# Kernel optimization log

Hardware: AMD Instinct MI355X
Metric: run time of the kernel (lower is better)

The kernel has to match this reference:

```python
import jax, jax.numpy as jnp
import numpy as np

Q_DIM, T_DIM, TOP_M, TEMP = 512, 768, 5, 0.07
B, H, W, K = 8, 64, 64, 128
LN_EPS = 1e-5

def _layernorm(x, g, b):
    mu = jnp.mean(x, axis=-1, keepdims=True)
    var = jnp.mean(jnp.square(x - mu), axis=-1, keepdims=True)
    return (x - mu) * jax.lax.rsqrt(var + LN_EPS) * g + b

def _l2norm(x):
    n = jnp.linalg.norm(x, axis=-1, keepdims=True)
    return x / jnp.maximum(n, 1e-12)

def setup_inputs() -> dict:
    key = jax.random.key(0)
    ks = jax.random.split(key, 12)
    s = lambda d: 1.0 / np.sqrt(d)
    return {
        'visual_features': jax.random.normal(ks[0], (B, H, W, Q_DIM), jnp.float32),
        'text_features': jax.random.normal(ks[1], (B, K, T_DIM), jnp.float32),
        'Wq': jax.random.uniform(ks[2], (Q_DIM, T_DIM), jnp.float32, -s(Q_DIM), s(Q_DIM)),
        'bq': jnp.zeros((T_DIM,), jnp.float32),
        'Wv': jax.random.uniform(ks[3], (T_DIM, Q_DIM), jnp.float32, -s(T_DIM), s(T_DIM)),
        'bv': jnp.zeros((Q_DIM,), jnp.float32),
        'W1': jax.random.uniform(ks[4], (Q_DIM, 4 * Q_DIM), jnp.float32, -s(Q_DIM), s(Q_DIM)),
        'b1': jnp.zeros((4 * Q_DIM,), jnp.float32),
        'W2': jax.random.uniform(ks[5], (4 * Q_DIM, Q_DIM), jnp.float32, -s(4 * Q_DIM), s(4 * Q_DIM)),
        'b2': jnp.zeros((Q_DIM,), jnp.float32),
        'g1': jnp.ones((Q_DIM,), jnp.float32), 'be1': jnp.zeros((Q_DIM,), jnp.float32),
        'g2': jnp.ones((Q_DIM,), jnp.float32), 'be2': jnp.zeros((Q_DIM,), jnp.float32),
    }

def reference(visual_features, text_features, Wq, bq, Wv, bv, W1, b1, W2, b2, g1, be1, g2, be2):
    b, h, w, c = visual_features.shape
    residual = visual_features.reshape(b, h * w, c)
    vis = _layernorm(residual, g1, be1)                      # (B,N,C)
    query = _l2norm(vis @ Wq + bq)                            # (B,N,Ct)
    keyt = _l2norm(text_features)                             # (B,K,Ct)
    value = text_features @ Wv + bv                           # (B,K,C)
    sim = jnp.einsum('bnc,bkc->bnk', query, keyt)             # (B,N,K)
    # top-M sparsification: keep top_m logits, others -> -inf
    top_v = jax.lax.top_k(sim, TOP_M)[0]                      # (B,N,M) sorted desc
    thr = top_v[..., -1:]
    sim = jnp.where(sim >= thr, sim, -jnp.inf)
    attn = jax.nn.softmax(sim / TEMP, axis=-1)
    aligned = jnp.einsum('bnk,bkc->bnc', attn, value)
    fused = residual + aligned
    fused = _layernorm(fused, g2, be2)
    ffn = jax.nn.gelu(fused @ W1 + b1, approximate=False) @ W2 + b2
    out = fused + ffn
    return out.reshape(b, h, w, c)
```

## Files before the change

### kernel.cpp

```cpp
#include <hip/hip_runtime.h>
#include <math.h>

typedef unsigned short u16;
typedef unsigned int   u32;
typedef unsigned long long u64;
typedef __attribute__((ext_vector_type(4))) float f32x4;
typedef __attribute__((ext_vector_type(4))) unsigned int u32x4;
typedef __attribute__((ext_vector_type(8))) _Float16 f16x8;

#define NROWS   32768
#define CDIM    512
#define TDIM    768
#define KKEY    128
#define FFDIM   2048
#define NB      8
#define RPB     4096
#define LN_EPS_ 1e-5f
#define TINV    (1.0f/0.07f)
#define RESCUE_MARGIN 1e-5f

__device__ __forceinline__ u16 f2h(float f){ _Float16 h=(_Float16)f; return __builtin_bit_cast(u16,h); }
__device__ __forceinline__ float h2f(u16 v){ return (float)__builtin_bit_cast(_Float16, v); }
__device__ __forceinline__ unsigned pk2(float a,float b){ return (unsigned)f2h(a)|((unsigned)f2h(b)<<16); }

__device__ __forceinline__ void gl_lds16(const void* g, void* l){
  __builtin_amdgcn_global_load_lds(
      (const __attribute__((address_space(1))) u32*)g,
      (__attribute__((address_space(3))) u32*)l, 16, 0, 0);
}

__device__ __forceinline__ float fast_exp2(float x){
#if __has_builtin(__builtin_amdgcn_exp2f)
  return __builtin_amdgcn_exp2f(x);
#else
  return exp2f(x);
#endif
}
__device__ __forceinline__ float fast_rcp(float x){
#if __has_builtin(__builtin_amdgcn_rcpf)
  return __builtin_amdgcn_rcpf(x);
#else
  return 1.0f/x;
#endif
}

__device__ __forceinline__ float wsumf(float v){
#pragma unroll
  for(int o=1;o<64;o<<=1) v+=__shfl_xor(v,o);
  return v; }
__device__ __forceinline__ float wmaxf(float v){
#pragma unroll
  for(int o=1;o<64;o<<=1) v=fmaxf(v,__shfl_xor(v,o));
  return v; }
__device__ __forceinline__ double wsumd(double v){
#pragma unroll
  for(int o=1;o<64;o<<=1) v+=__shfl_xor(v,o);
  return v; }
__device__ __forceinline__ double wmaxd(double v){
#pragma unroll
  for(int o=1;o<64;o<<=1){ double t=__shfl_xor(v,o); v = t>v ? t : v; }
  return v; }

__device__ __forceinline__ double blocksumd4(double v, double* red){
  const int lane = threadIdx.x & 63, w = threadIdx.x >> 6;
  v = wsumd(v);
  __syncthreads();
  if (lane==0) red[w] = v;
  __syncthreads();
  return red[0]+red[1]+red[2]+red[3];
}

template<int R, int C, bool F16>
__device__ __forceinline__ void tr_tile(const float* __restrict__ in, void* __restrict__ out,
                                        int bx, int by, float (*tile)[33])
{
  int c0 = bx*32, r0 = by*32;
  int tx = threadIdx.x, ty = threadIdx.y;
#pragma unroll
  for (int i=0;i<4;i++){
    int r = r0 + ty + i*8;
    tile[ty+i*8][tx] = in[(size_t)r*C + c0 + tx];
  }
  __syncthreads();
#pragma unroll
  for (int i=0;i<4;i++){
    int cc = c0 + ty + i*8, rr = r0 + tx;
    float v = tile[tx][ty+i*8];
    if (F16) ((u16*)out)[(size_t)cc*R + rr] = f2h(v);
    else     ((float*)out)[(size_t)cc*R + rr] = v;
  }
}

__global__ __launch_bounds__(256) void transpose_all_kernel(
    const float* __restrict__ Wq, const float* __restrict__ W1,
    const float* __restrict__ W2, const float* __restrict__ Wv,
    u16* __restrict__ Wq16t, u16* __restrict__ W116t,
    u16* __restrict__ W216t, float* __restrict__ WvT)
{
  __shared__ float tile[32][33];
  int bid = blockIdx.x;
  if (bid < 384){
    tr_tile<512,768,true>(Wq, Wq16t, bid%24, bid/24, tile);
  } else if (bid < 1408){
    int b = bid-384;  tr_tile<512,2048,true>(W1, W116t, b%64, b/64, tile);
  } else if (bid < 2432){
    int b = bid-1408; tr_tile<2048,512,true>(W2, W216t, b%16, b/16, tile);
  } else {
    int b = bid-2432; tr_tile<768,512,false>(Wv, WvT, b%16, b/16, tile);
  }
}

__global__ __launch_bounds__(256) void keystats_kernel(
    const float* __restrict__ text, const float* __restrict__ bq,
    float* __restrict__ normk, float* __restrict__ crr)
{
  int gw = blockIdx.x*4 + (threadIdx.x>>6);
  int lane = threadIdx.x & 63;
  const float* tr = &text[(size_t)gw*TDIM];
  double ss=0.0, db=0.0;
#pragma unroll
  for (int i=0;i<12;i++){
    float v = tr[lane + 64*i];
    ss += (double)v*(double)v;
    db += (double)bq[lane+64*i]*(double)v;
  }
  ss = wsumd(ss); db = wsumd(db);
  if (lane==0){
    double nk = sqrt(ss); nk = nk>1e-12 ? nk : 1e-12;
    normk[gw] = (float)nk;
    crr[gw]   = (float)db;
  }
}

__global__ __launch_bounds__(256) void ln1_kernel(
    const float* __restrict__ visual, const float* __restrict__ g1, const float* __restrict__ be1,
    float2* __restrict__ musig, u16* __restrict__ vis16)
{
  int row = blockIdx.x*4 + (threadIdx.x>>6);
  int lane = threadIdx.x & 63;
  size_t base = (size_t)row*CDIM + lane*8;
  f32x4 a = *(const f32x4*)&visual[base];
  f32x4 c = *(const f32x4*)&visual[base+4];
  float s = a[0]+a[1]+a[2]+a[3]+c[0]+c[1]+c[2]+c[3];
  s = wsumf(s);
  float mu = s * (1.0f/512.0f);
  float q = 0.f;
#pragma unroll
  for (int i=0;i<4;i++){ float d=a[i]-mu; q+=d*d; }
#pragma unroll
  for (int i=0;i<4;i++){ float d=c[i]-mu; q+=d*d; }
  q = wsumf(q);
  float rs = rsqrtf(q*(1.0f/512.0f) + LN_EPS_);
  int cb = lane*8;
  f32x4 o0,o1;
#pragma unroll
  for (int i=0;i<4;i++) o0[i] = (a[i]-mu)*rs*g1[cb+i]   + be1[cb+i];
#pragma unroll
  for (int i=0;i<4;i++) o1[i] = (c[i]-mu)*rs*g1[cb+4+i] + be1[cb+4+i];
  u32x4 hv;
  hv[0]=pk2(o0[0],o0[1]); hv[1]=pk2(o0[2],o0[3]);
  hv[2]=pk2(o1[0],o1[1]); hv[3]=pk2(o1[2],o1[3]);
  *(u32x4*)&vis16[base] = hv;
  if (lane==0){ float2 ms; ms.x=mu; ms.y=rs; musig[row]=ms; }
}

template<bool LNA>
__global__ __launch_bounds__(256) void gemm_f32_kernel(
    const float* __restrict__ A, const float* __restrict__ Bt, float* __restrict__ C,
    int M, int N, int K, long sA, long sB, long sC,
    const float2* __restrict__ musig, const float* __restrict__ g1, const float* __restrict__ be1)
{
  __shared__ float As[64][17];
  __shared__ float Bs[64][17];
  const int z = blockIdx.z;
  A  += (size_t)z * sA; Bt += (size_t)z * sB; C += (size_t)z * sC;
  const int tid = threadIdx.x;
  const int tx = tid & 15, ty = tid >> 4;
  const int m0 = blockIdx.x*64, n0 = blockIdx.y*64;
  float acc[4][4];
#pragma unroll
  for (int i=0;i<4;i++)
#pragma unroll
    for (int j=0;j<4;j++) acc[i][j]=0.f;
  const int lr = tid >> 2, lc = (tid & 3)*4;
  float2 ms;
  if (LNA) ms = musig[(size_t)z*M + m0 + lr];
  for (int k0=0; k0<K; k0+=16){
    f32x4 av = *(const f32x4*)&A [(size_t)(m0+lr)*K + k0 + lc];
    f32x4 bv = *(const f32x4*)&Bt[(size_t)(n0+lr)*K + k0 + lc];
    if (LNA){
      f32x4 gv  = *(const f32x4*)&g1[k0+lc];
      f32x4 bev = *(const f32x4*)&be1[k0+lc];
#pragma unroll
      for (int i=0;i<4;i++) av[i] = (av[i]-ms.x)*ms.y*gv[i] + bev[i];
    }
#pragma unroll
    for (int i=0;i<4;i++){ As[lr][lc+i]=av[i]; Bs[lr][lc+i]=bv[i]; }
    __syncthreads();
#pragma unroll
    for (int kk=0; kk<16; kk++){
      float a[4], b[4];
#pragma unroll
      for (int i=0;i<4;i++){ a[i]=As[ty*4+i][kk]; b[i]=Bs[tx*4+i][kk]; }
#pragma unroll
      for (int i=0;i<4;i++)
#pragma unroll
        for (int j=0;j<4;j++) acc[i][j] = fmaf(a[i], b[j], acc[i][j]);
    }
    __syncthreads();
  }
#pragma unroll
  for (int i=0;i<4;i++){
    f32x4 o;
#pragma unroll
    for (int j=0;j<4;j++) o[j]=acc[i][j];
    *(f32x4*)&C[(size_t)(m0+ty*4+i)*N + n0 + tx*4] = o;
  }
}

__device__ __forceinline__ float gelu_exact(float v){
  float x  = v*0.70710678118654752440f;
  float ax = fabsf(x);
  float t  = fast_rcp(fmaf(0.3275911f, ax, 1.0f));
  float p  = t*fmaf(t, fmaf(t, fmaf(t, fmaf(t, 1.061405429f, -1.453152027f),
                  1.421413741f), -0.284496736f), 0.254829592f);
  float e  = fast_exp2(ax*ax*(-1.4426950408889634f));
  float y  = 1.0f - p*e;
  float er = (x < 0.0f) ? -y : y;
  return 0.5f*v*(1.0f + er);
}

template<int EPI, int NN, int KK, int NT>
__global__ __launch_bounds__(256) void gemm_f16_kernel(
    const u16* __restrict__ A, const u16* __restrict__ Bt,
    const float* __restrict__ bias,
    float* __restrict__ out_f,
    u16* __restrict__ out_h,
    const u16* __restrict__ add_h)
{
  __shared__ __align__(16) u16 As[128*64];
  __shared__ __align__(16) u16 Bs[128*64];
  const int tid = threadIdx.x;
  const int lane = tid & 63, w = tid >> 6;
  const int wr = w >> 1, wc = w & 1;
  constexpr int NWG = 256*NT;
  const int wg = blockIdx.x;
  const int b2 = (wg & 7)*(NWG/8) + (wg >> 3);
  const int ntile = b2 % NT, mtile = b2 / NT;
  const int m0 = mtile*128, n0 = ntile*128;
  f32x4 acc[4][4];
#pragma unroll
  for (int i=0;i<4;i++)
#pragma unroll
    for (int j=0;j<4;j++) acc[i][j] = (f32x4)0.f;
  const int lr = lane & 15, lk = (lane >> 4)*8;
  const int c8_sw = ((lane & 7) ^ (lane >> 3))*8;
  const size_t stride32 = (size_t)32*KK;
  const u16* aptr = &A [(size_t)(m0 + w*8 + (lane>>3))*KK + c8_sw];
  const u16* bptr = &Bt[(size_t)(n0 + w*8 + (lane>>3))*KK + c8_sw];
  for (int k0=0; k0<KK; k0+=64){
#pragma unroll
    for (int i=0;i<4;i++){
      gl_lds16(aptr + i*stride32, &As[w*512 + i*2048]);
      gl_lds16(bptr + i*stride32, &Bs[w*512 + i*2048]);
    }
    aptr += 64; bptr += 64;
    __syncthreads();
#pragma unroll
    for (int kk=0; kk<64; kk+=32){
      f16x8 af[4], bfv[4];
      const int csw = (kk + lk) ^ ((lr & 7) << 3);
#pragma unroll
      for (int mi=0;mi<4;mi++) af[mi]  = *(const f16x8*)&As[(wr*64 + mi*16 + lr)*64 + csw];
#pragma unroll
      for (int ni=0;ni<4;ni++) bfv[ni] = *(const f16x8*)&Bs[(wc*64 + ni*16 + lr)*64 + csw];
#pragma unroll
      for (int mi=0;mi<4;mi++)
#pragma unroll
        for (int ni=0;ni<4;ni++)
          acc[mi][ni] = __builtin_amdgcn_mfma_f32_16x16x32_f16(af[mi], bfv[ni], acc[mi][ni], 0, 0, 0);
    }
    __syncthreads();
  }
  const int lr4 = (lane >> 4)*4;
  if (EPI == 0){
    float sq[4][4];
#pragma unroll
    for (int mi=0;mi<4;mi++)
#pragma unroll
      for (int r=0;r<4;r++) sq[mi][r]=0.f;
#pragma unroll
    for (int ni=0;ni<4;ni++){
      float bqv = bias[n0 + wc*64 + ni*16 + lr];
#pragma unroll
      for (int mi=0;mi<4;mi++)
#pragma unroll
        for (int r=0;r<4;r++){
          float v = acc[mi][ni][r] + bqv;
          sq[mi][r] += v*v;
        }
    }
#pragma unroll
    for (int o=1;o<16;o<<=1)
#pragma unroll
      for (int mi=0;mi<4;mi++)
#pragma unroll
        for (int r=0;r<4;r++) sq[mi][r] += __shfl_xor(sq[mi][r], o);
    if ((lane & 15) == 0){
      int part = ntile*2 + wc;
#pragma unroll
      for (int mi=0;mi<4;mi++)
#pragma unroll
        for (int r=0;r<4;r++){
          int row = m0 + wr*64 + mi*16 + lr4 + r;
          out_f[(size_t)row*12 + part] = sq[mi][r];
        }
    }
  } else {
    const int row0 = m0 + wr*64 + lr4;
    const int col0 = n0 + wc*64 + lr;
    float bb[4];
#pragma unroll
    for (int ni=0;ni<4;ni++) bb[ni] = bias[col0 + ni*16];
    if (EPI == 1){
      u16* op = out_h + (size_t)row0*NN + col0;
#pragma unroll
      for (int mi=0;mi<4;mi++)
#pragma unroll
        for (int r=0;r<4;r++)
#pragma unroll
          for (int ni=0;ni<4;ni++)
            op[(size_t)(mi*16+r)*NN + ni*16] = f2h(gelu_exact(acc[mi][ni][r] + bb[ni]));
    } else {
      float* op = out_f + (size_t)row0*NN + col0;
      const u16* rp = add_h + (size_t)row0*NN + col0;
#pragma unroll
      for (int mi=0;mi<4;mi++)
#pragma unroll
        for (int r=0;r<4;r++)
#pragma unroll
          for (int ni=0;ni<4;ni++)
            op[(size_t)(mi*16+r)*NN + ni*16] =
                acc[mi][ni][r] + bb[ni] + h2f(rp[(size_t)(mi*16+r)*NN + ni*16]);
    }
  }
}

__global__ __launch_bounds__(256) void rescue_kernel(
    const int* __restrict__ rcnt, const int* __restrict__ rlist,
    const float* __restrict__ visual, const float* __restrict__ text,
    const float* __restrict__ Wq, const float* __restrict__ bq,
    const float* __restrict__ g1, const float* __restrict__ be1,
    const float* __restrict__ g2, const float* __restrict__ be2,
    const float* __restrict__ value, const float* __restrict__ bv,
    u16* __restrict__ fused16)
{
  __shared__ double vis64[512];
  __shared__ double q64[768];
  __shared__ double sims[128];
  __shared__ double pw[128];
  __shared__ double red[4];
  __shared__ double sc2[2];
  __shared__ int klist[128];
  __shared__ int kcount;
  const int tid = threadIdx.x, lane = tid & 63, w = tid >> 6;
  int n = *rcnt; if (n > NROWS) n = NROWS;
  for (int i = blockIdx.x; i < n; i += gridDim.x){
    const int row = rlist[i], b = row >> 12;
    const size_t rb = (size_t)row*CDIM;
    double x0 = (double)visual[rb+tid], x1 = (double)visual[rb+tid+256];
    double s = blocksumd4(x0+x1, red);
    double mu = s*(1.0/512.0);
    double d0 = x0-mu, d1 = x1-mu;
    double var = blocksumd4(d0*d0+d1*d1, red);
    double rs = 1.0/sqrt(var*(1.0/512.0) + 1e-5);
    vis64[tid]     = d0*rs*(double)g1[tid]     + (double)be1[tid];
    vis64[tid+256] = d1*rs*(double)g1[tid+256] + (double)be1[tid+256];
    __syncthreads();
    double qa0=(double)bq[tid], qa1=(double)bq[tid+256], qa2=(double)bq[tid+512];
#pragma unroll 4
    for (int c=0;c<CDIM;c++){
      double v = vis64[c];
      const float* wrow = &Wq[(size_t)c*TDIM];
      qa0 += v*(double)wrow[tid];
      qa1 += v*(double)wrow[tid+256];
      qa2 += v*(double)wrow[tid+512];
    }
    q64[tid]=qa0; q64[tid+256]=qa1; q64[tid+512]=qa2;
    double nq2 = blocksumd4(qa0*qa0+qa1*qa1+qa2*qa2, red);
    double nq = sqrt(nq2); if (nq < 1e-12) nq = 1e-12;
    __syncthreads();
    if (tid < KKEY){
      const float* trow = &text[((size_t)b*KKEY + tid)*TDIM];
      double dot=0.0, nk2=0.0;
#pragma unroll 8
      for (int j=0;j<TDIM;j++){
        double tv = (double)trow[j];
        dot += q64[j]*tv; nk2 += tv*tv;
      }
      double nk = sqrt(nk2); if (nk < 1e-12) nk = 1e-12;
      sims[tid] = dot/(nq*nk);
    }
    __syncthreads();
    if (w == 0){
      double v0=sims[lane], v1=sims[lane+64];
      bool rm0=false, rm1=false;
      double thr=0.0, smax=0.0;
      for (int it=0; it<5; ++it){
        double c0 = rm0 ? -1e300 : v0;
        double c1 = rm1 ? -1e300 : v1;
        double m = wmaxd(c0>c1 ? c0 : c1);
        if (it==0) smax = m;
        thr = m;
        bool h0 = (!rm0) && (v0==m);
        u64 k0 = __ballot(h0);
        if (k0){ if (lane == __ffsll(k0)-1) rm0 = true; }
        else {
          bool h1 = (!rm1) && (v1==m);
          u64 k1 = __ballot(h1);
          if (lane == __ffsll(k1)-1) rm1 = true;
        }
      }
      if (lane==0){ sc2[0]=smax; sc2[1]=thr; kcount=0; }
    }
    __syncthreads();
    const double smax = sc2[0], thr = sc2[1];
    double p = 0.0;
    if (tid < KKEY){
      double sv = sims[tid];
      p = (sv >= thr) ? exp((sv-smax)*(1.0/0.07)) : 0.0;
      pw[tid] = p;
      if (p > 0.0){ int pos = atomicAdd(&kcount, 1); klist[pos] = tid; }
    }
    double Z = blocksumd4(p, red);
    double zi = 1.0/Z;
    __syncthreads();
    double a0=(double)bv[tid], a1=(double)bv[tid+256];
    int kc = kcount;
    for (int ki=0; ki<kc; ++ki){
      int k = klist[ki];
      double wt = pw[k]*zi;
      const float* vr = &value[((size_t)b*KKEY + k)*CDIM];
      a0 += wt*(double)vr[tid];
      a1 += wt*(double)vr[tid+256];
    }
    double f0 = (double)visual[rb+tid]     + a0;
    double f1 = (double)visual[rb+tid+256] + a1;
    double fsum = blocksumd4(f0+f1, red);
    double fmu = fsum*(1.0/512.0);
    double e0=f0-fmu, e1=f1-fmu;
    double fvar = blocksumd4(e0*e0+e1*e1, red);
    double frs = 1.0/sqrt(fvar*(1.0/512.0) + 1e-5);
    fused16[rb+tid]     = f2h((float)(e0*frs*(double)g2[tid]     + (double)be2[tid]));
    fused16[rb+tid+256] = f2h((float)(e1*frs*(double)g2[tid+256] + (double)be2[tid+256]));
    __syncthreads();
  }
}

__global__ __launch_bounds__(256) void attn_ln2_kernel(
    const float* __restrict__ visual,
    const float* __restrict__ tbuf, const float* __restrict__ crr,
    const float* __restrict__ normk, const float* __restrict__ qpart,
    const float* __restrict__ value, const float* __restrict__ bv,
    const float* __restrict__ g2, const float* __restrict__ be2,
    u16* __restrict__ fused16,
    int* __restrict__ rcnt, int* __restrict__ rlist)
{
  const int w = threadIdx.x >> 6, lane = threadIdx.x & 63;
  const int row = blockIdx.x*4 + w;
  const int b = row >> 12;
  float nqp = (lane < 12) ? qpart[(size_t)row*12 + lane] : 0.f;
  float nq2 = wsumf(nqp);
  float nq = fmaxf(sqrtf(nq2), 1e-12f);
  const float* trow = &tbuf[(size_t)row*KKEY];
  float s0 = (trow[lane]    + crr[b*KKEY + lane])    / (nq*normk[b*KKEY + lane]);
  float s1 = (trow[lane+64] + crr[b*KKEY + lane+64]) / (nq*normk[b*KKEY + lane+64]);
  float v0=s0, v1=s1; bool rm0=false, rm1=false;
  float thr=0.f, smax=0.f, m6=0.f;
  for (int it=0; it<6; ++it){
    float c0 = rm0 ? -1e30f : v0;
    float c1 = rm1 ? -1e30f : v1;
    float m = wmaxf(fmaxf(c0,c1));
    if (it==0) smax = m;
    if (it<5){
      thr = m;
      bool h0 = (!rm0) && (v0==m);
      u64 k0 = __ballot(h0);
      if (k0){ if (lane == __ffsll(k0)-1) rm0 = true; }
      else {
        bool h1 = (!rm1) && (v1==m);
        u64 k1 = __ballot(h1);
        if (lane == __ffsll(k1)-1) rm1 = true;
      }
    } else m6 = m;
  }
  if ((thr - m6) < RESCUE_MARGIN){
    if (lane == 0){
      int p = atomicAdd(rcnt, 1);
      rlist[p] = row;
    }
    return;
  }
  float p0 = (s0>=thr) ? expf((s0-smax)*TINV) : 0.f;
  float p1 = (s1>=thr) ? expf((s1-smax)*TINV) : 0.f;
  float Z = wsumf(p0+p1);
  float zi = 1.f/Z;
  float accv[8];
#pragma unroll
  for (int j=0;j<8;j++) accv[j] = bv[lane*8+j];
  u64 mk0 = __ballot(p0>0.f);
  u64 mk1 = __ballot(p1>0.f);
  while (mk0){
    int l = __ffsll(mk0)-1; mk0 &= mk0-1;
    float wt = __shfl(p0, l)*zi;
    const f32x4* vr = (const f32x4*)&value[((size_t)b*KKEY + l)*CDIM + lane*8];
    f32x4 va = vr[0], vb = vr[1];
#pragma unroll
    for (int j=0;j<4;j++){ accv[j] += wt*va[j]; accv[4+j] += wt*vb[j]; }
  }
  while (mk1){
    int l = __ffsll(mk1)-1; mk1 &= mk1-1;
    float wt = __shfl(p1, l)*zi;
    const f32x4* vr = (const f32x4*)&value[((size_t)b*KKEY + l + 64)*CDIM + lane*8];
    f32x4 va = vr[0], vb = vr[1];
#pragma unroll
    for (int j=0;j<4;j++){ accv[j] += wt*va[j]; accv[4+j] += wt*vb[j]; }
  }
  size_t rb = (size_t)row*CDIM + lane*8;
  f32x4 r0v = *(const f32x4*)&visual[rb];
  f32x4 r1v = *(const f32x4*)&visual[rb+4];
  float f[8];
#pragma unroll
  for (int j=0;j<4;j++){ f[j]=r0v[j]+accv[j]; f[4+j]=r1v[j]+accv[4+j]; }
  float fs=0.f;
#pragma unroll
  for (int j=0;j<8;j++) fs += f[j];
  fs = wsumf(fs);
  float fmu = fs*(1.0f/512.0f);
  float fvv=0.f;
#pragma unroll
  for (int j=0;j<8;j++){ float d=f[j]-fmu; fvv+=d*d; }
  fvv = wsumf(fvv);
  float frs = rsqrtf(fvv*(1.0f/512.0f) + LN_EPS_);
  int cb = lane*8;
  f32x4 o0,o1;
#pragma unroll
  for (int j=0;j<4;j++) o0[j] = (f[j]-fmu)*frs*g2[cb+j]     + be2[cb+j];
#pragma unroll
  for (int j=0;j<4;j++) o1[j] = (f[4+j]-fmu)*frs*g2[cb+4+j] + be2[cb+4+j];
  u32x4 hv;
  hv[0]=pk2(o0[0],o0[1]); hv[1]=pk2(o0[2],o0[3]);
  hv[2]=pk2(o1[0],o1[1]); hv[3]=pk2(o1[2],o1[3]);
  *(u32x4*)&fused16[rb] = hv;
}

extern "C" void kernel_launch(void* const* d_in, const int* in_sizes, int n_in,
                              void* d_out, int out_size, void* d_ws, size_t ws_size,
                              hipStream_t stream)
{
  (void)in_sizes; (void)n_in; (void)out_size; (void)ws_size;
  const float* visual = (const float*)d_in[0];
  const float* text   = (const float*)d_in[1];
  const float* Wq     = (const float*)d_in[2];
  const float* bq     = (const float*)d_in[3];
  const float* Wv     = (const float*)d_in[4];
  const float* bv     = (const float*)d_in[5];
  const float* W1     = (const float*)d_in[6];
  const float* b1     = (const float*)d_in[7];
  const float* W2     = (const float*)d_in[8];
  const float* b2     = (const float*)d_in[9];
  const float* g1     = (const float*)d_in[10];
  const float* be1    = (const float*)d_in[11];
  const float* g2     = (const float*)d_in[12];
  const float* be2    = (const float*)d_in[13];
  float* out = (float*)d_out;

  char* ws = (char*)d_ws;
  size_t off = 0;
  auto alloc = [&](size_t bytes)->char*{
    char* p = ws + off; off += (bytes + 255) & ~(size_t)255; return p; };

  u16*    vis16  = (u16*)   alloc((size_t)NROWS*CDIM*2);
  u16*    h16    = (u16*)   alloc((size_t)NROWS*FFDIM*2);
  float*  tbuf   = (float*) alloc((size_t)NROWS*KKEY*4);
  float*  Mrt    = (float*) alloc((size_t)NB*KKEY*CDIM*4);
  float*  value  = (float*) alloc((size_t)NB*KKEY*CDIM*4);
  u16*    Wq16t  = (u16*)   alloc((size_t)TDIM*CDIM*2);
  u16*    W116t  = (u16*)   alloc((size_t)FFDIM*CDIM*2);
  u16*    W216t  = (u16*)   alloc((size_t)CDIM*FFDIM*2);
  float*  WvT    = (float*) alloc((size_t)CDIM*TDIM*4);
  float*  qpart  = (float*) alloc((size_t)NROWS*12*4);
  float*  normk  = (float*) alloc((size_t)NB*KKEY*4);
  float*  crr    = (float*) alloc((size_t)NB*KKEY*4);
  float2* musig  = (float2*)alloc((size_t)NROWS*8);
  int*    rcnt   = (int*)   alloc(256);
  int*    rlist  = (int*)   alloc((size_t)NROWS*4);
  u16*    fused16 = vis16;

  hipMemsetAsync(rcnt, 0, sizeof(int), stream);

  transpose_all_kernel<<<2816, dim3(32,8), 0, stream>>>(
      Wq, W1, W2, Wv, Wq16t, W116t, W216t, WvT);
  keystats_kernel<<<256, 256, 0, stream>>>(text, bq, normk, crr);
  gemm_f32_kernel<false><<<dim3(2, 8, 8), 256, 0, stream>>>(
      text, Wq, Mrt, KKEY, CDIM, TDIM, (long)KKEY*TDIM, 0, (long)KKEY*CDIM,
      nullptr, nullptr, nullptr);
  gemm_f32_kernel<false><<<dim3(2, 8, 8), 256, 0, stream>>>(
      text, WvT, value, KKEY, CDIM, TDIM, (long)KKEY*TDIM, 0, (long)KKEY*CDIM,
      nullptr, nullptr, nullptr);
  ln1_kernel<<<NROWS/4, 256, 0, stream>>>(visual, g1, be1, musig, vis16);
  gemm_f32_kernel<true><<<dim3(64, 2, 8), 256, 0, stream>>>(
      visual, Mrt, tbuf, RPB, KKEY, CDIM, (long)RPB*CDIM, (long)KKEY*CDIM, (long)RPB*KKEY,
      musig, g1, be1);
  gemm_f16_kernel<0,TDIM,CDIM,6><<<1536, 256, 0, stream>>>(
      vis16, Wq16t, bq, qpart, nullptr, nullptr);
  attn_ln2_kernel<<<NROWS/4, 256, 0, stream>>>(
      visual, tbuf, crr, normk, qpart, value, bv, g2, be2,
      fused16, rcnt, rlist);
  rescue_kernel<<<256, 256, 0, stream>>>(
      rcnt, rlist, visual, text, Wq, bq, g1, be1, g2, be2, value, bv, fused16);
  gemm_f16_kernel<1,FFDIM,CDIM,16><<<4096, 256, 0, stream>>>(
      fused16, W116t, b1, nullptr, h16, nullptr);
  gemm_f16_kernel<2,CDIM,FFDIM,4><<<1024, 256, 0, stream>>>(
      h16, W216t, b2, out, nullptr, fused16);
}
```

Baseline: 565.7 us.

## Replace FP32 similarity GEMM with split-bf16 MFMA GEMM and double-buffer f16 GEMMs

The similarity GEMM (visual × Mrt) moves from a scalar FP32 SIMT kernel with LN applied on the fly to a bf16 MFMA kernel. It emulates FP32 precision by splitting LN1 output and Mrt into hi/lo bf16 parts and accumulating hi·hi, hi·lo and lo·hi over three passes. LN1 now writes bf16 hi/lo planes, Wq is converted to bf16, and the q-projection GEMM runs bf16 MFMA. The shared f16 GEMM kernel gains double-buffered LDS staging with explicit vmcnt waits to overlap global loads with MFMA. This adds workspace and extra memory traffic for the lo planes, and it risks small precision changes near top-k thresholds.

New measurement: 514.7 us. -9.0%, faster.

```diff
diff --git a/kernel.cpp b/kernel.cpp
--- a/kernel.cpp
+++ b/kernel.cpp
@@ -7,6 +7,7 @@
 typedef __attribute__((ext_vector_type(4))) float f32x4;
 typedef __attribute__((ext_vector_type(4))) unsigned int u32x4;
 typedef __attribute__((ext_vector_type(8))) _Float16 f16x8;
+typedef __attribute__((ext_vector_type(8))) short s16x8;
 
 #define NROWS   32768
 #define CDIM    512
@@ -22,6 +23,13 @@
 __device__ __forceinline__ u16 f2h(float f){ _Float16 h=(_Float16)f; return __builtin_bit_cast(u16,h); }
 __device__ __forceinline__ float h2f(u16 v){ return (float)__builtin_bit_cast(_Float16, v); }
 __device__ __forceinline__ unsigned pk2(float a,float b){ return (unsigned)f2h(a)|((unsigned)f2h(b)<<16); }
+__device__ __forceinline__ u16 f2b(float f){
+  u32 u = __builtin_bit_cast(u32, f);
+  u32 r = (u + 0x7fffu + ((u>>16)&1u)) >> 16;
+  return (u16)r;
+}
+__device__ __forceinline__ float b2f(u16 h){ u32 u = ((u32)h)<<16; return __builtin_bit_cast(float, u); }
+__device__ __forceinline__ unsigned pkb(float a,float b){ return (unsigned)f2b(a)|((unsigned)f2b(b)<<16); }
 
 __device__ __forceinline__ void gl_lds16(const void* g, void* l){
   __builtin_amdgcn_global_load_lds(
@@ -70,7 +78,7 @@
   return red[0]+red[1]+red[2]+red[3];
 }
 
-template<int R, int C, bool F16>
+template<int R, int C, int MODE>
 __device__ __forceinline__ void tr_tile(const float* __restrict__ in, void* __restrict__ out,
                                         int bx, int by, float (*tile)[33])
 {
@@ -86,27 +94,28 @@
   for (int i=0;i<4;i++){
     int cc = c0 + ty + i*8, rr = r0 + tx;
     float v = tile[tx][ty+i*8];
-    if (F16) ((u16*)out)[(size_t)cc*R + rr] = f2h(v);
-    else     ((float*)out)[(size_t)cc*R + rr] = v;
+    if (MODE==1)      ((u16*)out)[(size_t)cc*R + rr] = f2h(v);
+    else if (MODE==2) ((u16*)out)[(size_t)cc*R + rr] = f2b(v);
+    else              ((float*)out)[(size_t)cc*R + rr] = v;
   }
 }
 
 __global__ __launch_bounds__(256) void transpose_all_kernel(
     const float* __restrict__ Wq, const float* __restrict__ W1,
     const float* __restrict__ W2, const float* __restrict__ Wv,
-    u16* __restrict__ Wq16t, u16* __restrict__ W116t,
+    u16* __restrict__ Wqbt, u16* __restrict__ W116t,
     u16* __restrict__ W216t, float* __restrict__ WvT)
 {
   __shared__ float tile[32][33];
   int bid = blockIdx.x;
   if (bid < 384){
-    tr_tile<512,768,true>(Wq, Wq16t, bid%24, bid/24, tile);
+    tr_tile<512,768,2>(Wq, Wqbt, bid%24, bid/24, tile);
   } else if (bid < 1408){
-    int b = bid-384;  tr_tile<512,2048,true>(W1, W116t, b%64, b/64, tile);
+    int b = bid-384;  tr_tile<512,2048,1>(W1, W116t, b%64, b/64, tile);
   } else if (bid < 2432){
-    int b = bid-1408; tr_tile<2048,512,true>(W2, W216t, b%16, b/16, tile);
+    int b = bid-1408; tr_tile<2048,512,1>(W2, W216t, b%16, b/16, tile);
   } else {
-    int b = bid-2432; tr_tile<768,512,false>(Wv, WvT, b%16, b/16, tile);
+    int b = bid-2432; tr_tile<768,512,0>(Wv, WvT, b%16, b/16, tile);
   }
 }
 
@@ -134,7 +143,7 @@
 
 __global__ __launch_bounds__(256) void ln1_kernel(
     const float* __restrict__ visual, const float* __restrict__ g1, const float* __restrict__ be1,
-    float2* __restrict__ musig, u16* __restrict__ vis16)
+    u16* __restrict__ visH, u16* __restrict__ visL)
 {
   int row = blockIdx.x*4 + (threadIdx.x>>6);
   int lane = threadIdx.x & 63;
@@ -152,23 +161,28 @@
   q = wsumf(q);
   float rs = rsqrtf(q*(1.0f/512.0f) + LN_EPS_);
   int cb = lane*8;
-  f32x4 o0,o1;
-#pragma unroll
-  for (int i=0;i<4;i++) o0[i] = (a[i]-mu)*rs*g1[cb+i]   + be1[cb+i];
-#pragma unroll
-  for (int i=0;i<4;i++) o1[i] = (c[i]-mu)*rs*g1[cb+4+i] + be1[cb+4+i];
-  u32x4 hv;
-  hv[0]=pk2(o0[0],o0[1]); hv[1]=pk2(o0[2],o0[3]);
-  hv[2]=pk2(o1[0],o1[1]); hv[3]=pk2(o1[2],o1[3]);
-  *(u32x4*)&vis16[base] = hv;
-  if (lane==0){ float2 ms; ms.x=mu; ms.y=rs; musig[row]=ms; }
-}
-
-template<bool LNA>
+  float o[8];
+#pragma unroll
+  for (int i=0;i<4;i++) o[i]   = (a[i]-mu)*rs*g1[cb+i]   + be1[cb+i];
+#pragma unroll
+  for (int i=0;i<4;i++) o[4+i] = (c[i]-mu)*rs*g1[cb+4+i] + be1[cb+4+i];
+  u16 hh[8];
+  float lo[8];
+#pragma unroll
+  for (int i=0;i<8;i++){ hh[i] = f2b(o[i]); lo[i] = o[i] - b2f(hh[i]); }
+  u32x4 hv, lv;
+#pragma unroll
+  for (int i=0;i<4;i++){
+    hv[i] = (u32)hh[2*i] | ((u32)hh[2*i+1]<<16);
+    lv[i] = pkb(lo[2*i], lo[2*i+1]);
+  }
+  *(u32x4*)&visH[base] = hv;
+  *(u32x4*)&visL[base] = lv;
+}
+
 __global__ __launch_bounds__(256) void gemm_f32_kernel(
     const float* __restrict__ A, const float* __restrict__ Bt, float* __restrict__ C,
-    int M, int N, int K, long sA, long sB, long sC,
-    const float2* __restrict__ musig, const float* __restrict__ g1, const float* __restrict__ be1)
+    int M, int N, int K, long sA, long sB, long sC)
 {
   __shared__ float As[64][17];
   __shared__ float Bs[64][17];
@@ -183,17 +197,9 @@
 #pragma unroll
     for (int j=0;j<4;j++) acc[i][j]=0.f;
   const int lr = tid >> 2, lc = (tid & 3)*4;
-  float2 ms;
-  if (LNA) ms = musig[(size_t)z*M + m0 + lr];
   for (int k0=0; k0<K; k0+=16){
     f32x4 av = *(const f32x4*)&A [(size_t)(m0+lr)*K + k0 + lc];
     f32x4 bv = *(const f32x4*)&Bt[(size_t)(n0+lr)*K + k0 + lc];
-    if (LNA){
-      f32x4 gv  = *(const f32x4*)&g1[k0+lc];
-      f32x4 bev = *(const f32x4*)&be1[k0+lc];
-#pragma unroll
-      for (int i=0;i<4;i++) av[i] = (av[i]-ms.x)*ms.y*gv[i] + bev[i];
-    }
 #pragma unroll
     for (int i=0;i<4;i++){ As[lr][lc+i]=av[i]; Bs[lr][lc+i]=bv[i]; }
     __syncthreads();
@@ -216,6 +222,23 @@
     for (int j=0;j<4;j++) o[j]=acc[i][j];
     *(f32x4*)&C[(size_t)(m0+ty*4+i)*N + n0 + tx*4] = o;
   }
+}
+
+__global__ __launch_bounds__(256) void split_kernel(
+    const float* __restrict__ in, u16* __restrict__ hi, u16* __restrict__ lo, int n4)
+{
+  int i = blockIdx.x*256 + threadIdx.x;
+  if (i >= n4) return;
+  f32x4 v = *(const f32x4*)&in[i*4];
+  u32 hw[2], lw[2];
+#pragma unroll
+  for (int j=0;j<2;j++){
+    u16 h0 = f2b(v[2*j]), h1 = f2b(v[2*j+1]);
+    hw[j] = (u32)h0 | ((u32)h1<<16);
+    lw[j] = pkb(v[2*j]-b2f(h0), v[2*j+1]-b2f(h1));
+  }
+  ((u32*)hi)[i*2]   = hw[0]; ((u32*)hi)[i*2+1] = hw[1];
+  ((u32*)lo)[i*2]   = lw[0]; ((u32*)lo)[i*2+1] = lw[1];
 }
 
 __device__ __forceinline__ float gelu_exact(float v){
@@ -238,8 +261,8 @@
     u16* __restrict__ out_h,
     const u16* __restrict__ add_h)
 {
-  __shared__ __align__(16) u16 As[128*64];
-  __shared__ __align__(16) u16 Bs[128*64];
+  __shared__ __align__(16) u16 As[2][128*64];
+  __shared__ __align__(16) u16 Bs[2][128*64];
   const int tid = threadIdx.x;
   const int lane = tid & 63, w = tid >> 6;
   const int wr = w >> 1, wc = w & 1;
@@ -256,31 +279,48 @@
   const int lr = lane & 15, lk = (lane >> 4)*8;
   const int c8_sw = ((lane & 7) ^ (lane >> 3))*8;
   const size_t stride32 = (size_t)32*KK;
-  const u16* aptr = &A [(size_t)(m0 + w*8 + (lane>>3))*KK + c8_sw];
-  const u16* bptr = &Bt[(size_t)(n0 + w*8 + (lane>>3))*KK + c8_sw];
+  const u16* aBase = &A [(size_t)(m0 + w*8 + (lane>>3))*KK + c8_sw];
+  const u16* bBase = &Bt[(size_t)(n0 + w*8 + (lane>>3))*KK + c8_sw];
+
+  auto STAGE = [&](int buf, int k0){
+#pragma unroll
+    for (int i=0;i<4;i++){
+      gl_lds16(aBase + i*stride32 + k0, &As[buf][w*512 + i*2048]);
+      gl_lds16(bBase + i*stride32 + k0, &Bs[buf][w*512 + i*2048]);
+    }
+  };
+
+  STAGE(0, 0);
+  int cur = 0;
   for (int k0=0; k0<KK; k0+=64){
-#pragma unroll
-    for (int i=0;i<4;i++){
-      gl_lds16(aptr + i*stride32, &As[w*512 + i*2048]);
-      gl_lds16(bptr + i*stride32, &Bs[w*512 + i*2048]);
-    }
-    aptr += 64; bptr += 64;
-    __syncthreads();
+    if (k0 + 64 < KK){
+      STAGE(cur^1, k0+64);
+      asm volatile("s_waitcnt vmcnt(8)" ::: "memory");
+    } else {
+      asm volatile("s_waitcnt vmcnt(0)" ::: "memory");
+    }
+    __builtin_amdgcn_s_barrier();
 #pragma unroll
     for (int kk=0; kk<64; kk+=32){
-      f16x8 af[4], bfv[4];
+      s16x8 af[4], bfv[4];
       const int csw = (kk + lk) ^ ((lr & 7) << 3);
 #pragma unroll
-      for (int mi=0;mi<4;mi++) af[mi]  = *(const f16x8*)&As[(wr*64 + mi*16 + lr)*64 + csw];
-#pragma unroll
-      for (int ni=0;ni<4;ni++) bfv[ni] = *(const f16x8*)&Bs[(wc*64 + ni*16 + lr)*64 + csw];
+      for (int mi=0;mi<4;mi++) af[mi]  = *(const s16x8*)&As[cur][(wr*64 + mi*16 + lr)*64 + csw];
+#pragma unroll
+      for (int ni=0;ni<4;ni++) bfv[ni] = *(const s16x8*)&Bs[cur][(wc*64 + ni*16 + lr)*64 + csw];
 #pragma unroll
       for (int mi=0;mi<4;mi++)
 #pragma unroll
-        for (int ni=0;ni<4;ni++)
-          acc[mi][ni] = __builtin_amdgcn_mfma_f32_16x16x32_f16(af[mi], bfv[ni], acc[mi][ni], 0, 0, 0);
-    }
-    __syncthreads();
+        for (int ni=0;ni<4;ni++){
+          if (EPI == 0)
+            acc[mi][ni] = __builtin_amdgcn_mfma_f32_16x16x32_bf16(af[mi], bfv[ni], acc[mi][ni], 0, 0, 0);
+          else
+            acc[mi][ni] = __builtin_amdgcn_mfma_f32_16x16x32_f16(
+                __builtin_bit_cast(f16x8, af[mi]), __builtin_bit_cast(f16x8, bfv[ni]), acc[mi][ni], 0, 0, 0);
+        }
+    }
+    __builtin_amdgcn_s_barrier();
+    cur ^= 1;
   }
   const int lr4 = (lane >> 4)*4;
   if (EPI == 0){
@@ -344,6 +384,80 @@
                 acc[mi][ni][r] + bb[ni] + h2f(rp[(size_t)(mi*16+r)*NN + ni*16]);
     }
   }
+}
+
+__global__ __launch_bounds__(256) void gemm_t_kernel(
+    const u16* __restrict__ Ah, const u16* __restrict__ Al,
+    const u16* __restrict__ Bh, const u16* __restrict__ Bl,
+    float* __restrict__ C)
+{
+  __shared__ __align__(16) u16 As[2][128*64];
+  __shared__ __align__(16) u16 Bs[2][128*64];
+  const int tid = threadIdx.x;
+  const int lane = tid & 63, w = tid >> 6;
+  const int wr = w >> 1, wc = w & 1;
+  const int mtile = blockIdx.x;
+  const int m0 = mtile*128, z = mtile >> 5;
+  f32x4 acc[4][4];
+#pragma unroll
+  for (int i=0;i<4;i++)
+#pragma unroll
+    for (int j=0;j<4;j++) acc[i][j] = (f32x4)0.f;
+  const int lr = lane & 15, lk = (lane >> 4)*8;
+  const int c8_sw = ((lane & 7) ^ (lane >> 3))*8;
+  const size_t aOff = (size_t)(m0 + w*8 + (lane>>3))*CDIM + c8_sw;
+  const size_t bOff = (size_t)(z*KKEY + w*8 + (lane>>3))*CDIM + c8_sw;
+  const size_t stride32 = (size_t)32*CDIM;
+
+  auto STAGE = [&](int buf, int s){
+    const int p = s >> 3, k0 = (s & 7) << 6;
+    const u16* Ap = (p==2) ? Al : Ah;
+    const u16* Bp = (p==1) ? Bl : Bh;
+#pragma unroll
+    for (int i=0;i<4;i++){
+      gl_lds16(Ap + aOff + i*stride32 + k0, &As[buf][w*512 + i*2048]);
+      gl_lds16(Bp + bOff + i*stride32 + k0, &Bs[buf][w*512 + i*2048]);
+    }
+  };
+
+  STAGE(0, 0);
+  int cur = 0;
+  for (int s=0; s<24; ++s){
+    if (s < 23){
+      STAGE(cur^1, s+1);
+      asm volatile("s_waitcnt vmcnt(8)" ::: "memory");
+    } else {
+      asm volatile("s_waitcnt vmcnt(0)" ::: "memory");
+    }
+    __builtin_amdgcn_s_barrier();
+#pragma unroll
+    for (int kk=0; kk<64; kk+=32){
+      s16x8 af[4], bfv[4];
+      const int csw = (kk + lk) ^ ((lr & 7) << 3);
+#pragma unroll
+      for (int mi=0;mi<4;mi++) af[mi]  = *(const s16x8*)&As[cur][(wr*64 + mi*16 + lr)*64 + csw];
+#pragma unroll
+      for (int ni=0;ni<4;ni++) bfv[ni] = *(const s16x8*)&Bs[cur][(wc*64 + ni*16 + lr)*64 + csw];
+#pragma unroll
+      for (int mi=0;mi<4;mi++)
+#pragma unroll
+        for (int ni=0;ni<4;ni++)
+          acc[mi][ni] = __builtin_amdgcn_mfma_f32_16x16x32_bf16(af[mi], bfv[ni], acc[mi][ni], 0, 0, 0);
+    }
+    __builtin_amdgcn_s_barrier();
+    cur ^= 1;
+  }
+  const int lr4 = (lane >> 4)*4;
+  const int row0 = m0 + wr*64 + lr4;
+  const int col0 = wc*64 + lr;
+  float* op = C + (size_t)row0*KKEY + col0;
+#pragma unroll
+  for (int mi=0;mi<4;mi++)
+#pragma unroll
+    for (int r=0;r<4;r++)
+#pragma unroll
+      for (int ni=0;ni<4;ni++)
+        op[(size_t)(mi*16+r)*KKEY + ni*16] = acc[mi][ni][r];
 }
 
 __global__ __launch_bounds__(256) void rescue_kernel(
@@ -580,40 +694,39 @@
   auto alloc = [&](size_t bytes)->char*{
     char* p = ws + off; off += (bytes + 255) & ~(size_t)255; return p; };
 
-  u16*    vis16  = (u16*)   alloc((size_t)NROWS*CDIM*2);
+  u16*    visH   = (u16*)   alloc((size_t)NROWS*CDIM*2);
+  u16*    visL   = (u16*)   alloc((size_t)NROWS*CDIM*2);
   u16*    h16    = (u16*)   alloc((size_t)NROWS*FFDIM*2);
+  u16*    fused16= (u16*)   alloc((size_t)NROWS*CDIM*2);
   float*  tbuf   = (float*) alloc((size_t)NROWS*KKEY*4);
   float*  Mrt    = (float*) alloc((size_t)NB*KKEY*CDIM*4);
+  u16*    MrtH   = (u16*)   alloc((size_t)NB*KKEY*CDIM*2);
+  u16*    MrtL   = (u16*)   alloc((size_t)NB*KKEY*CDIM*2);
   float*  value  = (float*) alloc((size_t)NB*KKEY*CDIM*4);
-  u16*    Wq16t  = (u16*)   alloc((size_t)TDIM*CDIM*2);
+  u16*    Wqbt   = (u16*)   alloc((size_t)TDIM*CDIM*2);
   u16*    W116t  = (u16*)   alloc((size_t)FFDIM*CDIM*2);
   u16*    W216t  = (u16*)   alloc((size_t)CDIM*FFDIM*2);
   float*  WvT    = (float*) alloc((size_t)CDIM*TDIM*4);
   float*  qpart  = (float*) alloc((size_t)NROWS*12*4);
   float*  normk  = (float*) alloc((size_t)NB*KKEY*4);
   float*  crr    = (float*) alloc((size_t)NB*KKEY*4);
-  float2* musig  = (float2*)alloc((size_t)NROWS*8);
   int*    rcnt   = (int*)   alloc(256);
   int*    rlist  = (int*)   alloc((size_t)NROWS*4);
-  u16*    fused16 = vis16;
 
   hipMemsetAsync(rcnt, 0, sizeof(int), stream);
 
   transpose_all_kernel<<<2816, dim3(32,8), 0, stream>>>(
-      Wq, W1, W2, Wv, Wq16t, W116t, W216t, WvT);
+      Wq, W1, W2, Wv, Wqbt, W116t, W216t, WvT);
   keystats_kernel<<<256, 256, 0, stream>>>(text, bq, normk, crr);
-  gemm_f32_kernel<false><<<dim3(2, 8, 8), 256, 0, stream>>>(
-      text, Wq, Mrt, KKEY, CDIM, TDIM, (long)KKEY*TDIM, 0, (long)KKEY*CDIM,
-      nullptr, nullptr, nullptr);
-  gemm_f32_kernel<false><<<dim3(2, 8, 8), 256, 0, stream>>>(
-      text, WvT, value, KKEY, CDIM, TDIM, (long)KKEY*TDIM, 0, (long)KKEY*CDIM,
-      nullptr, nullptr, nullptr);
-  ln1_kernel<<<NROWS/4, 256, 0, stream>>>(visual, g1, be1, musig, vis16);
-  gemm_f32_kernel<true><<<dim3(64, 2, 8), 256, 0, stream>>>(
-      visual, Mrt, tbuf, RPB, KKEY, CDIM, (long)RPB*CDIM, (long)KKEY*CDIM, (long)RPB*KKEY,
-      musig, g1, be1);
+  gemm_f32_kernel<<<dim3(2, 8, 8), 256, 0, stream>>>(
+      text, Wq, Mrt, KKEY, CDIM, TDIM, (long)KKEY*TDIM, 0, (long)KKEY*CDIM);
+  gemm_f32_kernel<<<dim3(2, 8, 8), 256, 0, stream>>>(
+      text, WvT, value, KKEY, CDIM, TDIM, (long)KKEY*TDIM, 0, (long)KKEY*CDIM);
+  split_kernel<<<512, 256, 0, stream>>>(Mrt, MrtH, MrtL, NB*KKEY*CDIM/4);
+  ln1_kernel<<<NROWS/4, 256, 0, stream>>>(visual, g1, be1, visH, visL);
+  gemm_t_kernel<<<256, 256, 0, stream>>>(visH, visL, MrtH, MrtL, tbuf);
   gemm_f16_kernel<0,TDIM,CDIM,6><<<1536, 256, 0, stream>>>(
-      vis16, Wq16t, bq, qpart, nullptr, nullptr);
+      visH, Wqbt, bq, qpart, nullptr, nullptr);
   attn_ln2_kernel<<<NROWS/4, 256, 0, stream>>>(
       visual, tbuf, crr, normk, qpart, value, bv, g2, be2,
       fused16, rcnt, rlist);
```
